# Kernel tuning notes

Hardware: AMD Instinct MI355X
Metric: run time of the kernel (lower is better)

The kernel has to match this reference:

```python
import jax, jax.numpy as jnp
import numpy as np

EPS = 1e-5
GROUPS = 8

def group_norm(x, w, b):
    B, C, H, W = x.shape
    xg = x.reshape(B, GROUPS, C // GROUPS, H, W)
    mean = xg.mean(axis=(2, 3, 4), keepdims=True)
    var = xg.var(axis=(2, 3, 4), keepdims=True)
    xn = ((xg - mean) * jax.lax.rsqrt(var + EPS)).reshape(B, C, H, W)
    return xn * w[None, :, None, None] + b[None, :, None, None]

def conv1x1(x, w, b):
    # x: [B,C,H,W], w: [O,C] -> [B,O,H,W]
    return jnp.einsum('bchw,oc->bohw', x, w) + b[None, :, None, None]

def setup_inputs() -> dict:
    key = jax.random.key(0)
    ks = jax.random.split(key, 16)
    C, Ci = 256, 128
    B, H, W = 4, 64, 64
    s3 = 1.0 / np.sqrt(C * 9)
    s1 = 1.0 / np.sqrt(C)
    return {
        'x': jax.random.normal(ks[0], (B, C, H, W), jnp.float32),
        'smooth_w': jax.random.uniform(ks[1], (C, C, 3, 3), jnp.float32, -s3, s3),
        'smooth_b': jax.random.uniform(ks[2], (C,), jnp.float32, -s3, s3),
        'gn1_w': jnp.ones((C,), jnp.float32),
        'gn1_b': jnp.zeros((C,), jnp.float32),
        'g_w': jax.random.uniform(ks[3], (Ci, C), jnp.float32, -s1, s1),
        'g_b': jax.random.uniform(ks[4], (Ci,), jnp.float32, -s1, s1),
        'theta_w': jax.random.uniform(ks[5], (Ci, C), jnp.float32, -s1, s1),
        'theta_b': jax.random.uniform(ks[6], (Ci,), jnp.float32, -s1, s1),
        'phi_w': jax.random.uniform(ks[7], (Ci, C), jnp.float32, -s1, s1),
        'phi_b': jax.random.uniform(ks[8], (Ci,), jnp.float32, -s1, s1),
        'w_w': 0.01 * jax.random.normal(ks[9], (C, Ci), jnp.float32),
        'w_b': jnp.zeros((C,), jnp.float32),
        'gn2_w': jnp.ones((C,), jnp.float32),
        'gn2_b': jnp.zeros((C,), jnp.float32),
    }

def reference(x, smooth_w, smooth_b, gn1_w, gn1_b, g_w, g_b, theta_w, theta_b,
              phi_w, phi_b, w_w, w_b, gn2_w, gn2_b):
    # input_smooth: 3x3 conv + GroupNorm(8) + ReLU
    xs = jax.lax.conv_general_dilated(
        x, smooth_w, window_strides=(1, 1), padding='SAME',
        dimension_numbers=('NCHW', 'OIHW', 'NCHW')) + smooth_b[None, :, None, None]
    xs = jax.nn.relu(group_norm(xs, gn1_w, gn1_b))
    B, C, H, W = xs.shape
    Ci = g_w.shape[0]
    N = H * W
    g_x = conv1x1(xs, g_w, g_b).reshape(B, Ci, N).transpose(0, 2, 1)      # [B,N,Ci]
    theta_x = conv1x1(xs, theta_w, theta_b).reshape(B, Ci, N).transpose(0, 2, 1)  # [B,N,Ci]
    phi_x = conv1x1(xs, phi_w, phi_b).reshape(B, Ci, N)                   # [B,Ci,N]
    f = jnp.einsum('bnc,bcm->bnm', theta_x, phi_x)                        # [B,N,N]
    attn = jax.nn.softmax(f, axis=-1)
    y = jnp.einsum('bnm,bmc->bnc', attn, g_x)                             # [B,N,Ci]
    y = y.transpose(0, 2, 1).reshape(B, Ci, H, W)
    w_y = group_norm(conv1x1(y, w_w, w_b), gn2_w, gn2_b)
    return w_y * 0.1 + xs
```

## Files before the change

### kernel.cpp

```cpp
#include <hip/hip_runtime.h>
#include <math.h>

#define Bn 4
#define Cn 256
#define CIn 128
#define Hn 64
#define Wn 64
#define Nn 4096
#define Gn 8
#define CPGn 32
#define EPSc 1e-5f

typedef unsigned short ushort_t;
typedef short bfrag __attribute__((ext_vector_type(8)));
typedef float f32x4 __attribute__((ext_vector_type(4)));
typedef ushort_t u16x8 __attribute__((ext_vector_type(8)));

static __device__ __forceinline__ ushort_t f2bf(float f) {
  unsigned u = __float_as_uint(f);
  return (ushort_t)((u + 0x7FFFu + ((u >> 16) & 1u)) >> 16);
}

static __device__ __forceinline__ unsigned cvt_pk_bf16(float lo, float hi) {
  unsigned r;
  asm("v_cvt_pk_bf16_f32 %0, %1, %2" : "=v"(r) : "v"(lo), "v"(hi));
  return r;
}

static __device__ __forceinline__ void gl_lds16(const ushort_t* g, ushort_t* l) {
  __builtin_amdgcn_global_load_lds(
      (__attribute__((address_space(1))) void*)g,
      (__attribute__((address_space(3))) void*)l, 16, 0, 0);
}

__global__ __launch_bounds__(256) void k_prepack(
    const float* __restrict__ w3, const float* __restrict__ thw,
    const float* __restrict__ phw, const float* __restrict__ gww,
    const float* __restrict__ ww,
    ushort_t* __restrict__ w9, ushort_t* __restrict__ wp9,
    ushort_t* __restrict__ wwb) {
  int i = blockIdx.x * 256 + threadIdx.x;
  if (i < 589824) {
    float v = w3[i];
    int co = i / 2304, r = i % 2304, ci = r / 9, tap = r % 9;
    w9[tap * 65536 + co * 256 + ci] = f2bf(v);
  } else if (i < 688128) {
    int j = i - 589824;
    int which = j >> 15, r = j & 32767;
    const float* src = (which == 0) ? thw : (which == 1) ? phw : gww;
    wp9[j] = f2bf(src[r]);
  } else if (i < 720896) {
    int j = i - 688128;
    wwb[j] = f2bf(ww[j]);
  }
}

__global__ __launch_bounds__(512) void k_conv_mfma(
    const float* __restrict__ x, const ushort_t* __restrict__ w9,
    const float* __restrict__ b3, float* __restrict__ out) {
  __shared__ __align__(16) ushort_t lx[3 * 66 * 128];
  const int tid = threadIdx.x;
  const int lane = tid & 63, w = tid >> 6;
  const int ln = lane & 15, lhi = lane >> 4;
  const int h = blockIdx.x, b = blockIdx.y;
  const int wco = w * 32;

  f32x4 acc[2][4];
#pragma unroll
  for (int mf = 0; mf < 2; ++mf)
#pragma unroll
    for (int nf = 0; nf < 4; ++nf) acc[mf][nf] = (f32x4){0.f, 0.f, 0.f, 0.f};

  for (int cc = 0; cc < 2; ++cc) {
    __syncthreads();
    for (int i = tid; i < 768; i += 512) {
      int dh = i / 256, r = i % 256, wpz = (r >> 7) ? 65 : 0, ci = r & 127;
      int off = (((dh * 66 + wpz) * 128 + ci) * 2) ^ ((wpz & 7) << 4);
      *(ushort_t*)((char*)lx + off) = 0;
    }
    for (int i = tid; i < 6144; i += 512) {
      int dh = i >> 11, r = i & 2047, ci = r >> 4, w4 = (r & 15) * 4;
      int hh = h + dh - 1;
      float4 v = {0.f, 0.f, 0.f, 0.f};
      if (hh >= 0 && hh < Hn)
        v = *(const float4*)(x + (((size_t)(b * Cn + cc * 128 + ci)) * Hn + hh) * Wn + w4);
      float vv[4] = {v.x, v.y, v.z, v.w};
#pragma unroll
      for (int j = 0; j < 4; ++j) {
        int wp = 1 + w4 + j;
        int off = (((dh * 66 + wp) * 128 + ci) * 2) ^ ((wp & 7) << 4);
        *(ushort_t*)((char*)lx + off) = f2bf(vv[j]);
      }
    }
    __syncthreads();

#pragma unroll
    for (int tap = 0; tap < 9; ++tap) {
      const int dh = tap / 3, dw = tap % 3;
#pragma unroll
      for (int kb = 0; kb < 4; ++kb) {
        const ushort_t* ap = w9 + tap * 65536 + (size_t)(wco + ln) * 256 +
                             cc * 128 + kb * 32 + lhi * 8;
        bfrag af0 = *(const bfrag*)ap;
        bfrag af1 = *(const bfrag*)(ap + 16 * 256);
        __builtin_amdgcn_s_setprio(1);
#pragma unroll
        for (int nf = 0; nf < 4; ++nf) {
          int wp = nf * 16 + ln + dw;
          int off = (((dh * 66 + wp) * 128 + kb * 32 + lhi * 8) * 2) ^ ((wp & 7) << 4);
          bfrag bf = *(const bfrag*)((const char*)lx + off);
          acc[0][nf] = __builtin_amdgcn_mfma_f32_16x16x32_bf16(af0, bf, acc[0][nf], 0, 0, 0);
          acc[1][nf] = __builtin_amdgcn_mfma_f32_16x16x32_bf16(af1, bf, acc[1][nf], 0, 0, 0);
        }
        __builtin_amdgcn_s_setprio(0);
      }
    }
  }

#pragma unroll
  for (int mf = 0; mf < 2; ++mf) {
    float4 bv = *(const float4*)(b3 + wco + mf * 16 + lhi * 4);
    float bb[4] = {bv.x, bv.y, bv.z, bv.w};
#pragma unroll
    for (int nf = 0; nf < 4; ++nf) {
#pragma unroll
      for (int r = 0; r < 4; ++r) {
        int co = wco + mf * 16 + lhi * 4 + r;
        out[((size_t)(b * Cn + co)) * Nn + h * Wn + nf * 16 + ln] = acc[mf][nf][r] + bb[r];
      }
    }
  }
}

__global__ __launch_bounds__(256) void k_gn_part(
    const float* __restrict__ xin, float* __restrict__ part) {
  const int s = blockIdx.x, g = blockIdx.y, b = blockIdx.z;
  const int t = threadIdx.x;
  const float* p = xin + ((size_t)b * Cn + g * CPGn) * Nn + s * 8192;
  float sum = 0.f, ssq = 0.f;
  for (int i = t * 4; i < 8192; i += 1024) {
    float4 v = *(const float4*)(p + i);
    sum += v.x + v.y + v.z + v.w;
    ssq += v.x * v.x + v.y * v.y + v.z * v.z + v.w * v.w;
  }
  __shared__ float r1[256], r2[256];
  r1[t] = sum; r2[t] = ssq;
  __syncthreads();
  for (int st = 128; st > 0; st >>= 1) {
    if (t < st) { r1[t] += r1[t + st]; r2[t] += r2[t + st]; }
    __syncthreads();
  }
  if (t == 0) {
    size_t idx = ((size_t)(b * Gn + g) * 16 + s) * 2;
    part[idx] = r1[0];
    part[idx + 1] = r2[0];
  }
}

__global__ void k_gn_final(const float* __restrict__ part, float* __restrict__ stats) {
  const int t = threadIdx.x;
  if (t < Bn * Gn) {
    float s = 0.f, ss = 0.f;
    for (int j = 0; j < 16; ++j) {
      s += part[(t * 16 + j) * 2];
      ss += part[(t * 16 + j) * 2 + 1];
    }
    const float inv = 1.f / (float)(CPGn * Nn);
    float mean = s * inv;
    float var = ss * inv - mean * mean;
    stats[t * 2] = mean;
    stats[t * 2 + 1] = rsqrtf(var + EPSc);
  }
}

__global__ __launch_bounds__(256) void k_gn1_apply_t(
    const float* __restrict__ xr, const float* __restrict__ stats,
    const float* __restrict__ gw, const float* __restrict__ gb,
    float* __restrict__ xs, ushort_t* __restrict__ xsT) {
  __shared__ ushort_t lt[32 * 64];
  const int t = threadIdx.x;
  const int n0 = blockIdx.x * 64, c0 = blockIdx.y * 32, b = blockIdx.z;
#pragma unroll
  for (int p = 0; p < 8; ++p) {
    int c = c0 + p * 4 + (t >> 6);
    int n = n0 + (t & 63);
    int bg = b * Gn + (c >> 5);
    float mean = stats[bg * 2], rstd = stats[bg * 2 + 1];
    float sc = gw[c] * rstd;
    float sb = gb[c] - mean * sc;
    size_t idx = ((size_t)(b * Cn + c)) * Nn + n;
    float val = fmaxf(xr[idx] * sc + sb, 0.f);
    xs[idx] = val;
    lt[(c - c0) * 64 + (t & 63)] = f2bf(val);
  }
  __syncthreads();
  {
    int n = t >> 2, cg = t & 3;
    u16x8 pk;
#pragma unroll
    for (int j = 0; j < 8; ++j) pk[j] = lt[(cg * 8 + j) * 64 + n];
    *(u16x8*)(xsT + ((size_t)(b * Nn + n0 + n)) * Cn + c0 + cg * 8) = pk;
  }
}

__global__ __launch_bounds__(256) void k_proj_mfma(
    const ushort_t* __restrict__ xsT, const ushort_t* __restrict__ wp9,
    const float* __restrict__ thb, const float* __restrict__ phb,
    const float* __restrict__ gbb,
    ushort_t* __restrict__ theta_b, ushort_t* __restrict__ phi_b,
    ushort_t* __restrict__ g_b) {
  __shared__ __align__(16) ushort_t lxs[64 * 256];
  const int tid = threadIdx.x;
  const int lane = tid & 63, w = tid >> 6;
  const int ln = lane & 15, lhi = lane >> 4;
  const int n0 = blockIdx.x * 64, which = blockIdx.y, b = blockIdx.z;
  const int wci = w * 32;

  for (int i = tid; i < 2048; i += 256) {
    int n = i >> 5, cchunk = (i & 31) * 8;
    uint4 v = *(const uint4*)(xsT + ((size_t)(b * Nn + n0 + n)) * Cn + cchunk);
    int off = ((n * 256 + cchunk) * 2) ^ ((n & 7) << 4);
    *(uint4*)((char*)lxs + off) = v;
  }
  __syncthreads();

  f32x4 acc[2][4];
#pragma unroll
  for (int mf = 0; mf < 2; ++mf)
#pragma unroll
    for (int nf = 0; nf < 4; ++nf) acc[mf][nf] = (f32x4){0.f, 0.f, 0.f, 0.f};

#pragma unroll
  for (int kb = 0; kb < 8; ++kb) {
    const ushort_t* ap = wp9 + which * 32768 + (size_t)(wci + ln) * 256 + kb * 32 + lhi * 8;
    bfrag af0 = *(const bfrag*)ap;
    bfrag af1 = *(const bfrag*)(ap + 16 * 256);
    __builtin_amdgcn_s_setprio(1);
#pragma unroll
    for (int nf = 0; nf < 4; ++nf) {
      int n = nf * 16 + ln;
      int off = ((n * 256 + kb * 32 + lhi * 8) * 2) ^ ((n & 7) << 4);
      bfrag bf = *(const bfrag*)((const char*)lxs + off);
      acc[0][nf] = __builtin_amdgcn_mfma_f32_16x16x32_bf16(af0, bf, acc[0][nf], 0, 0, 0);
      acc[1][nf] = __builtin_amdgcn_mfma_f32_16x16x32_bf16(af1, bf, acc[1][nf], 0, 0, 0);
    }
    __builtin_amdgcn_s_setprio(0);
  }

  const float* bs = (which == 0) ? thb : (which == 1) ? phb : gbb;
#pragma unroll
  for (int mf = 0; mf < 2; ++mf) {
    float4 bv = *(const float4*)(bs + wci + mf * 16 + lhi * 4);
    float bb[4] = {bv.x, bv.y, bv.z, bv.w};
    if (which < 2) {
      ushort_t* ob = ((which == 0) ? theta_b : phi_b) + (size_t)b * Nn * CIn;
#pragma unroll
      for (int nf = 0; nf < 4; ++nf) {
        int n = n0 + nf * 16 + ln;
        unsigned lo = (unsigned)f2bf(acc[mf][nf][0] + bb[0]) |
                      ((unsigned)f2bf(acc[mf][nf][1] + bb[1]) << 16);
        unsigned hi = (unsigned)f2bf(acc[mf][nf][2] + bb[2]) |
                      ((unsigned)f2bf(acc[mf][nf][3] + bb[3]) << 16);
        ushort_t* base = ob + (size_t)n * CIn + wci + mf * 16 + lhi * 4;
        *(unsigned*)base = lo;
        *(unsigned*)(base + 2) = hi;
      }
    } else {
      ushort_t* ob = g_b + (size_t)b * CIn * Nn;
#pragma unroll
      for (int nf = 0; nf < 4; ++nf) {
#pragma unroll
        for (int r = 0; r < 4; ++r) {
          int ci = wci + mf * 16 + lhi * 4 + r;
          ob[(size_t)ci * Nn + n0 + nf * 16 + ln] = f2bf(acc[mf][nf][r] + bb[r]);
        }
      }
    }
  }
}

__global__ __launch_bounds__(256) void k_attn_split(
    const ushort_t* __restrict__ theta_b, const ushort_t* __restrict__ phi_b,
    const ushort_t* __restrict__ g_b, ushort_t* __restrict__ ypart,
    float* __restrict__ mpart, float* __restrict__ lpart) {
  __shared__ __align__(16) ushort_t lphi[64 * 128];
  __shared__ __align__(16) ushort_t lg[128 * 64];
  __shared__ __align__(16) ushort_t lP[4][16 * 64];

  const int tid = threadIdx.x;
  const int lane = tid & 63, w = tid >> 6;
  const int ln = lane & 15, lhi = lane >> 4;

  const int bid = blockIdx.x;
  const int xcd = bid & 7, idx = bid >> 3;
  const int pair = xcd * 2 + (idx >> 6);
  const int b = pair >> 2, s = pair & 3;
  const int n0 = (idx & 63) * 64;
  const int kv0 = s * 1024;

  bfrag qf[4];
  {
    const ushort_t* thp =
        theta_b + ((size_t)(b * Nn + n0 + w * 16 + ln)) * CIn + 8 * lhi;
#pragma unroll
    for (int kb = 0; kb < 4; ++kb) qf[kb] = *(const bfrag*)(thp + kb * 32);
  }

  f32x4 yacc[8];
#pragma unroll
  for (int df = 0; df < 8; ++df) yacc[df] = (f32x4){0.f, 0.f, 0.f, 0.f};
  float mq = -3e38f, lq = 0.f;

  const ushort_t* gphi[4];
  const ushort_t* gg[4];
  ushort_t* ldphi[4];
  ushort_t* ldg[4];
#pragma unroll
  for (int k = 0; k < 4; ++k) {
    int ch = w * 4 + k;
    int boff = ch * 1024 + lane * 16;
    {
      int m = boff >> 8, c = (boff >> 4) & 15, cp = c ^ (m & 7);
      gphi[k] = phi_b + (size_t)b * Nn * CIn + (size_t)(kv0 + m) * CIn + cp * 8;
      ldphi[k] = lphi + ch * 512;
    }
    {
      int d = boff >> 7, c = (boff >> 4) & 7, cp = c ^ (d & 7);
      gg[k] = g_b + (size_t)b * CIn * Nn + (size_t)d * Nn + kv0 + cp * 8;
      ldg[k] = lg + ch * 512;
    }
  }
#pragma unroll
  for (int k = 0; k < 4; ++k) {
    gl_lds16(gphi[k], ldphi[k]);
    gl_lds16(gg[k], ldg[k]);
  }

  ushort_t* lPw = lP[w];

  for (int t = 0; t < 16; ++t) {
    __syncthreads();

    f32x4 sacc[4];
#pragma unroll
    for (int nf = 0; nf < 4; ++nf) sacc[nf] = (f32x4){0.f, 0.f, 0.f, 0.f};
    __builtin_amdgcn_s_setprio(1);
#pragma unroll
    for (int kb = 0; kb < 4; ++kb) {
#pragma unroll
      for (int nf = 0; nf < 4; ++nf) {
        int row = nf * 16 + ln;
        int off = ((row * 128 + kb * 32 + 8 * lhi) * 2) ^ ((ln & 7) << 4);
        bfrag pf = *(const bfrag*)((const char*)lphi + off);
        sacc[nf] = __builtin_amdgcn_mfma_f32_16x16x32_bf16(pf, qf[kb], sacc[nf], 0, 0, 0);
      }
    }
    __builtin_amdgcn_s_setprio(0);

    float mx;
    {
      float a0 = fmaxf(fmaxf(sacc[0][0], sacc[0][1]), fmaxf(sacc[0][2], sacc[0][3]));
      float a1 = fmaxf(fmaxf(sacc[1][0], sacc[1][1]), fmaxf(sacc[1][2], sacc[1][3]));
      float a2 = fmaxf(fmaxf(sacc[2][0], sacc[2][1]), fmaxf(sacc[2][2], sacc[2][3]));
      float a3 = fmaxf(fmaxf(sacc[3][0], sacc[3][1]), fmaxf(sacc[3][2], sacc[3][3]));
      mx = fmaxf(fmaxf(a0, a1), fmaxf(a2, a3));
    }
    mx = fmaxf(mx, __shfl_xor(mx, 16));
    mx = fmaxf(mx, __shfl_xor(mx, 32));
    float nm = fmaxf(mq, mx);
    float aaq = __expf(mq - nm);
    mq = nm;

    float psum = 0.f;
#pragma unroll
    for (int nf = 0; nf < 4; ++nf) {
      float p0 = __expf(sacc[nf][0] - nm);
      float p1 = __expf(sacc[nf][1] - nm);
      float p2 = __expf(sacc[nf][2] - nm);
      float p3 = __expf(sacc[nf][3] - nm);
      psum += (p0 + p1) + (p2 + p3);
      uint2 pk;
      pk.x = cvt_pk_bf16(p0, p1);
      pk.y = cvt_pk_bf16(p2, p3);
      int off = ((ln * 64 + nf * 16 + lhi * 4) * 2) ^ ((ln & 7) << 4);
      *(uint2*)((char*)lPw + off) = pk;
    }
    psum += __shfl_xor(psum, 16);
    psum += __shfl_xor(psum, 32);
    lq = lq * aaq + psum;

    float aar[4];
#pragma unroll
    for (int r = 0; r < 4; ++r) aar[r] = __shfl(aaq, 4 * lhi + r);
#pragma unroll
    for (int df = 0; df < 8; ++df)
#pragma unroll
      for (int r = 0; r < 4; ++r) yacc[df][r] *= aar[r];

    __builtin_amdgcn_s_setprio(1);
#pragma unroll
    for (int kb2 = 0; kb2 < 2; ++kb2) {
      int offa = ((ln * 64 + kb2 * 32 + 8 * lhi) * 2) ^ ((ln & 7) << 4);
      bfrag pa = *(const bfrag*)((const char*)lPw + offa);
#pragma unroll
      for (int df = 0; df < 8; ++df) {
        int d = df * 16 + ln;
        int offb = ((d * 64 + kb2 * 32 + 8 * lhi) * 2) ^ ((ln & 7) << 4);
        bfrag gbf = *(const bfrag*)((const char*)lg + offb);
        yacc[df] = __builtin_amdgcn_mfma_f32_16x16x32_bf16(pa, gbf, yacc[df], 0, 0, 0);
      }
    }
    __builtin_amdgcn_s_setprio(0);

    __syncthreads();
    if (t < 15) {
#pragma unroll
      for (int k = 0; k < 4; ++k) {
        gphi[k] += 64 * CIn;
        gg[k] += 64;
        gl_lds16(gphi[k], ldphi[k]);
        gl_lds16(gg[k], ldg[k]);
      }
    }
  }

  {
    ushort_t* ly = lphi;
#pragma unroll
    for (int df = 0; df < 8; ++df) {
#pragma unroll
      for (int r = 0; r < 4; ++r) {
        int q = w * 16 + lhi * 4 + r;
        int off = ((q * 128 + df * 16 + ln) * 2) ^ ((q & 7) << 4);
        *(ushort_t*)((char*)ly + off) = f2bf(yacc[df][r]);
      }
    }
  }
  __syncthreads();
  {
    int q = tid >> 2, c0 = (tid & 3) * 32;
    ushort_t* yp = ypart + ((size_t)((b * 4 + s) * Nn + n0 + q)) * CIn + c0;
#pragma unroll
    for (int k = 0; k < 4; ++k) {
      int off = ((q * 128 + c0 + k * 8) * 2) ^ ((q & 7) << 4);
      uint4 v = *(const uint4*)((const char*)lphi + off);
      *(uint4*)(yp + k * 8) = v;
    }
  }
  if (lhi == 0) {
    size_t qi = (size_t)(b * 4 + s) * Nn + n0 + w * 16 + ln;
    mpart[qi] = mq;
    lpart[qi] = lq;
  }
}

__global__ __launch_bounds__(256) void k_merge(
    const ushort_t* __restrict__ ypart, const float* __restrict__ mpart,
    const float* __restrict__ lpart, ushort_t* __restrict__ yT) {
  const int t = threadIdx.x;
  const int n = blockIdx.x * 64 + (t >> 2);
  const int b = blockIdx.y;
  const int d0 = (t & 3) * 32;
  float m[4], l[4];
#pragma unroll
  for (int s = 0; s < 4; ++s) {
    m[s] = mpart[(size_t)(b * 4 + s) * Nn + n];
    l[s] = lpart[(size_t)(b * 4 + s) * Nn + n];
  }
  float M = fmaxf(fmaxf(m[0], m[1]), fmaxf(m[2], m[3]));
  float L = 0.f, sc[4];
#pragma unroll
  for (int s = 0; s < 4; ++s) { sc[s] = __expf(m[s] - M); L += sc[s] * l[s]; }
  float inv = 1.f / L;
  float acc[32];
#pragma unroll
  for (int k = 0; k < 32; ++k) acc[k] = 0.f;
#pragma unroll
  for (int s = 0; s < 4; ++s) {
    const ushort_t* yp = ypart + ((size_t)((b * 4 + s) * Nn + n)) * CIn + d0;
#pragma unroll
    for (int k = 0; k < 4; ++k) {
      u16x8 v = *(const u16x8*)(yp + k * 8);
#pragma unroll
      for (int j = 0; j < 8; ++j)
        acc[k * 8 + j] += sc[s] * __uint_as_float((unsigned)v[j] << 16);
    }
  }
  ushort_t* op = yT + ((size_t)(b * Nn + n)) * CIn + d0;
#pragma unroll
  for (int k = 0; k < 4; ++k) {
    u16x8 pk;
#pragma unroll
    for (int j = 0; j < 8; ++j) pk[j] = f2bf(acc[k * 8 + j] * inv);
    *(u16x8*)(op + k * 8) = pk;
  }
}

__global__ __launch_bounds__(512) void k_wconv_mfma(
    const ushort_t* __restrict__ yT, const ushort_t* __restrict__ wwb,
    const float* __restrict__ wb, float* __restrict__ wy) {
  __shared__ __align__(16) ushort_t lyt[64 * 128];
  const int tid = threadIdx.x;
  const int lane = tid & 63, w = tid >> 6;
  const int ln = lane & 15, lhi = lane >> 4;
  const int n0 = blockIdx.x * 64, b = blockIdx.y;
  const int wco = w * 32;

  for (int i = tid; i < 1024; i += 512) {
    int n = i >> 4, ch = (i & 15) * 8;
    uint4 v = *(const uint4*)(yT + ((size_t)(b * Nn + n0 + n)) * CIn + ch);
    int off = ((n * 128 + ch) * 2) ^ ((n & 7) << 4);
    *(uint4*)((char*)lyt + off) = v;
  }
  __syncthreads();

  f32x4 acc[2][4];
#pragma unroll
  for (int mf = 0; mf < 2; ++mf)
#pragma unroll
    for (int nf = 0; nf < 4; ++nf) acc[mf][nf] = (f32x4){0.f, 0.f, 0.f, 0.f};

#pragma unroll
  for (int kb = 0; kb < 4; ++kb) {
    const ushort_t* ap = wwb + (size_t)(wco + ln) * CIn + kb * 32 + lhi * 8;
    bfrag af0 = *(const bfrag*)ap;
    bfrag af1 = *(const bfrag*)(ap + 16 * CIn);
    __builtin_amdgcn_s_setprio(1);
#pragma unroll
    for (int nf = 0; nf < 4; ++nf) {
      int n = nf * 16 + ln;
      int off = ((n * 128 + kb * 32 + lhi * 8) * 2) ^ ((n & 7) << 4);
      bfrag bf = *(const bfrag*)((const char*)lyt + off);
      acc[0][nf] = __builtin_amdgcn_mfma_f32_16x16x32_bf16(af0, bf, acc[0][nf], 0, 0, 0);
      acc[1][nf] = __builtin_amdgcn_mfma_f32_16x16x32_bf16(af1, bf, acc[1][nf], 0, 0, 0);
    }
    __builtin_amdgcn_s_setprio(0);
  }

#pragma unroll
  for (int mf = 0; mf < 2; ++mf) {
    float4 bv = *(const float4*)(wb + wco + mf * 16 + lhi * 4);
    float bb[4] = {bv.x, bv.y, bv.z, bv.w};
#pragma unroll
    for (int nf = 0; nf < 4; ++nf) {
#pragma unroll
      for (int r = 0; r < 4; ++r) {
        int co = wco + mf * 16 + lhi * 4 + r;
        wy[((size_t)(b * Cn + co)) * Nn + n0 + nf * 16 + ln] = acc[mf][nf][r] + bb[r];
      }
    }
  }
}

__global__ __launch_bounds__(256) void k_final(
    const float* __restrict__ wy, const float* __restrict__ stats,
    const float* __restrict__ g2w, const float* __restrict__ g2b,
    const float* __restrict__ xs, float* __restrict__ out) {
  size_t i = ((size_t)blockIdx.x * 256 + threadIdx.x) * 4;
  int c = (int)((i >> 12) & 255);
  int bg = (int)(i >> 20) * Gn + (c >> 5);
  float mean = stats[bg * 2], rstd = stats[bg * 2 + 1];
  float sc = g2w[c] * rstd * 0.1f;
  float sb = (g2b[c] - mean * rstd * g2w[c]) * 0.1f;
  float4 v = *(const float4*)(wy + i);
  float4 xv = *(const float4*)(xs + i);
  v.x = v.x * sc + sb + xv.x;
  v.y = v.y * sc + sb + xv.y;
  v.z = v.z * sc + sb + xv.z;
  v.w = v.w * sc + sb + xv.w;
  *(float4*)(out + i) = v;
}

extern "C" void kernel_launch(void* const* d_in, const int* in_sizes, int n_in,
                              void* d_out, int out_size, void* d_ws, size_t ws_size,
                              hipStream_t stream) {
  (void)in_sizes; (void)n_in; (void)out_size; (void)ws_size;
  const float* x   = (const float*)d_in[0];
  const float* sw  = (const float*)d_in[1];
  const float* sb  = (const float*)d_in[2];
  const float* g1w = (const float*)d_in[3];
  const float* g1b = (const float*)d_in[4];
  const float* gw  = (const float*)d_in[5];
  const float* gb  = (const float*)d_in[6];
  const float* thw = (const float*)d_in[7];
  const float* thb = (const float*)d_in[8];
  const float* phw = (const float*)d_in[9];
  const float* phb = (const float*)d_in[10];
  const float* ww  = (const float*)d_in[11];
  const float* wb  = (const float*)d_in[12];
  const float* g2w = (const float*)d_in[13];
  const float* g2b = (const float*)d_in[14];
  float* out = (float*)d_out;
  float* ws = (float*)d_ws;

  float*    xs_raw  = ws;
  float*    xs      = ws + 4194304;
  ushort_t* yT      = (ushort_t*)(ws + 8388608);
  float*    part    = ws + 10485760;
  float*    st1     = ws + 10486784;
  float*    st2     = ws + 10486848;
  ushort_t* theta_b = (ushort_t*)(ws + 10486912);
  ushort_t* phi_b   = (ushort_t*)(ws + 11535488);
  ushort_t* g_b     = (ushort_t*)(ws + 12584064);
  ushort_t* xsT     = (ushort_t*)(ws + 13632640);
  ushort_t* w9      = (ushort_t*)(ws + 15729792);
  ushort_t* wp9     = (ushort_t*)(ws + 16024704);
  ushort_t* wwb     = (ushort_t*)(ws + 16073856);
  ushort_t* ypart   = (ushort_t*)xs_raw;
  float*    mpart   = (float*)xsT;
  float*    lpart   = ((float*)xsT) + 65536;
  float*    wy      = xs_raw;

  k_prepack<<<2816, 256, 0, stream>>>(sw, thw, phw, gw, ww, w9, wp9, wwb);
  k_conv_mfma<<<dim3(Hn, Bn), 512, 0, stream>>>(x, w9, sb, xs_raw);
  k_gn_part<<<dim3(16, 8, 4), 256, 0, stream>>>(xs_raw, part);
  k_gn_final<<<1, 64, 0, stream>>>(part, st1);
  k_gn1_apply_t<<<dim3(64, 8, 4), 256, 0, stream>>>(xs_raw, st1, g1w, g1b, xs, xsT);
  k_proj_mfma<<<dim3(64, 3, 4), 256, 0, stream>>>(xsT, wp9, thb, phb, gb,
                                                  theta_b, phi_b, g_b);
  k_attn_split<<<1024, 256, 0, stream>>>(theta_b, phi_b, g_b, ypart, mpart, lpart);
  k_merge<<<dim3(64, 4), 256, 0, stream>>>(ypart, mpart, lpart, yT);
  k_wconv_mfma<<<dim3(64, 4), 512, 0, stream>>>(yT, wwb, wb, wy);
  k_gn_part<<<dim3(16, 8, 4), 256, 0, stream>>>(wy, part);
  k_gn_final<<<1, 64, 0, stream>>>(part, st2);
  k_final<<<4096, 256, 0, stream>>>(wy, st2, g2w, g2b, xs, out);
}
```

Measured before the change: 181.9 us.

## Fuse GroupNorm partial stats into conv epilogues and merge into wconv

Group-norm partial sums and sums of squares are now computed in the epilogues of the 3x3 conv and the output 1x1 conv, using wave shuffles. This removes the two separate k_gn_part passes that re-read full fp32 activations. The flash-split merge kernel is folded into k_wconv_mfma, which combines the four bf16 partial outputs with softmax rescale factors while staging into LDS, so the yT round trip goes away. Buffers are reassigned in the workspace to avoid aliasing, and k_gn_final now reduces 64 partials per group instead of 16.

Result: faster. 168.1 us (median of 2 runs) (-7.6%).

```diff
diff --git a/kernel.cpp b/kernel.cpp
--- a/kernel.cpp
+++ b/kernel.cpp
@@ -25,6 +25,10 @@
   unsigned r;
   asm("v_cvt_pk_bf16_f32 %0, %1, %2" : "=v"(r) : "v"(lo), "v"(hi));
   return r;
+}
+
+static __device__ __forceinline__ float bf2f(ushort_t u) {
+  return __uint_as_float((unsigned)u << 16);
 }
 
 static __device__ __forceinline__ void gl_lds16(const ushort_t* g, ushort_t* l) {
@@ -57,7 +61,8 @@
 
 __global__ __launch_bounds__(512) void k_conv_mfma(
     const float* __restrict__ x, const ushort_t* __restrict__ w9,
-    const float* __restrict__ b3, float* __restrict__ out) {
+    const float* __restrict__ b3, float* __restrict__ out,
+    float* __restrict__ part) {
   __shared__ __align__(16) ushort_t lx[3 * 66 * 128];
   const int tid = threadIdx.x;
   const int lane = tid & 63, w = tid >> 6;
@@ -117,6 +122,7 @@
     }
   }
 
+  float s_ = 0.f, q_ = 0.f;
 #pragma unroll
   for (int mf = 0; mf < 2; ++mf) {
     float4 bv = *(const float4*)(b3 + wco + mf * 16 + lhi * 4);
@@ -126,34 +132,22 @@
 #pragma unroll
       for (int r = 0; r < 4; ++r) {
         int co = wco + mf * 16 + lhi * 4 + r;
-        out[((size_t)(b * Cn + co)) * Nn + h * Wn + nf * 16 + ln] = acc[mf][nf][r] + bb[r];
-      }
-    }
-  }
-}
-
-__global__ __launch_bounds__(256) void k_gn_part(
-    const float* __restrict__ xin, float* __restrict__ part) {
-  const int s = blockIdx.x, g = blockIdx.y, b = blockIdx.z;
-  const int t = threadIdx.x;
-  const float* p = xin + ((size_t)b * Cn + g * CPGn) * Nn + s * 8192;
-  float sum = 0.f, ssq = 0.f;
-  for (int i = t * 4; i < 8192; i += 1024) {
-    float4 v = *(const float4*)(p + i);
-    sum += v.x + v.y + v.z + v.w;
-    ssq += v.x * v.x + v.y * v.y + v.z * v.z + v.w * v.w;
-  }
-  __shared__ float r1[256], r2[256];
-  r1[t] = sum; r2[t] = ssq;
-  __syncthreads();
-  for (int st = 128; st > 0; st >>= 1) {
-    if (t < st) { r1[t] += r1[t + st]; r2[t] += r2[t + st]; }
-    __syncthreads();
-  }
-  if (t == 0) {
-    size_t idx = ((size_t)(b * Gn + g) * 16 + s) * 2;
-    part[idx] = r1[0];
-    part[idx + 1] = r2[0];
+        float v = acc[mf][nf][r] + bb[r];
+        out[((size_t)(b * Cn + co)) * Nn + h * Wn + nf * 16 + ln] = v;
+        s_ += v;
+        q_ += v * v;
+      }
+    }
+  }
+#pragma unroll
+  for (int off = 32; off; off >>= 1) {
+    s_ += __shfl_xor(s_, off);
+    q_ += __shfl_xor(q_, off);
+  }
+  if (lane == 0) {
+    size_t pi = ((size_t)(b * Gn + w) * 64 + h) * 2;
+    part[pi] = s_;
+    part[pi + 1] = q_;
   }
 }
 
@@ -161,9 +155,9 @@
   const int t = threadIdx.x;
   if (t < Bn * Gn) {
     float s = 0.f, ss = 0.f;
-    for (int j = 0; j < 16; ++j) {
-      s += part[(t * 16 + j) * 2];
-      ss += part[(t * 16 + j) * 2 + 1];
+    for (int j = 0; j < 64; ++j) {
+      s += part[(t * 64 + j) * 2];
+      ss += part[(t * 64 + j) * 2 + 1];
     }
     const float inv = 1.f / (float)(CPGn * Nn);
     float mean = s * inv;
@@ -454,63 +448,55 @@
   }
 }
 
-__global__ __launch_bounds__(256) void k_merge(
+__global__ __launch_bounds__(512) void k_wconv_mfma(
     const ushort_t* __restrict__ ypart, const float* __restrict__ mpart,
-    const float* __restrict__ lpart, ushort_t* __restrict__ yT) {
-  const int t = threadIdx.x;
-  const int n = blockIdx.x * 64 + (t >> 2);
-  const int b = blockIdx.y;
-  const int d0 = (t & 3) * 32;
-  float m[4], l[4];
-#pragma unroll
-  for (int s = 0; s < 4; ++s) {
-    m[s] = mpart[(size_t)(b * 4 + s) * Nn + n];
-    l[s] = lpart[(size_t)(b * 4 + s) * Nn + n];
-  }
-  float M = fmaxf(fmaxf(m[0], m[1]), fmaxf(m[2], m[3]));
-  float L = 0.f, sc[4];
-#pragma unroll
-  for (int s = 0; s < 4; ++s) { sc[s] = __expf(m[s] - M); L += sc[s] * l[s]; }
-  float inv = 1.f / L;
-  float acc[32];
-#pragma unroll
-  for (int k = 0; k < 32; ++k) acc[k] = 0.f;
-#pragma unroll
-  for (int s = 0; s < 4; ++s) {
-    const ushort_t* yp = ypart + ((size_t)((b * 4 + s) * Nn + n)) * CIn + d0;
-#pragma unroll
-    for (int k = 0; k < 4; ++k) {
-      u16x8 v = *(const u16x8*)(yp + k * 8);
-#pragma unroll
-      for (int j = 0; j < 8; ++j)
-        acc[k * 8 + j] += sc[s] * __uint_as_float((unsigned)v[j] << 16);
-    }
-  }
-  ushort_t* op = yT + ((size_t)(b * Nn + n)) * CIn + d0;
-#pragma unroll
-  for (int k = 0; k < 4; ++k) {
-    u16x8 pk;
-#pragma unroll
-    for (int j = 0; j < 8; ++j) pk[j] = f2bf(acc[k * 8 + j] * inv);
-    *(u16x8*)(op + k * 8) = pk;
-  }
-}
-
-__global__ __launch_bounds__(512) void k_wconv_mfma(
-    const ushort_t* __restrict__ yT, const ushort_t* __restrict__ wwb,
-    const float* __restrict__ wb, float* __restrict__ wy) {
+    const float* __restrict__ lpart, const ushort_t* __restrict__ wwb,
+    const float* __restrict__ wb, float* __restrict__ wy,
+    float* __restrict__ part) {
   __shared__ __align__(16) ushort_t lyt[64 * 128];
+  __shared__ float fSc[4][64];
   const int tid = threadIdx.x;
   const int lane = tid & 63, w = tid >> 6;
   const int ln = lane & 15, lhi = lane >> 4;
   const int n0 = blockIdx.x * 64, b = blockIdx.y;
   const int wco = w * 32;
 
+  if (tid < 64) {
+    int n = n0 + tid;
+    float m0 = mpart[(size_t)(b * 4 + 0) * Nn + n], l0 = lpart[(size_t)(b * 4 + 0) * Nn + n];
+    float m1 = mpart[(size_t)(b * 4 + 1) * Nn + n], l1 = lpart[(size_t)(b * 4 + 1) * Nn + n];
+    float m2 = mpart[(size_t)(b * 4 + 2) * Nn + n], l2 = lpart[(size_t)(b * 4 + 2) * Nn + n];
+    float m3 = mpart[(size_t)(b * 4 + 3) * Nn + n], l3 = lpart[(size_t)(b * 4 + 3) * Nn + n];
+    float M = fmaxf(fmaxf(m0, m1), fmaxf(m2, m3));
+    float s0 = __expf(m0 - M), s1 = __expf(m1 - M), s2 = __expf(m2 - M), s3 = __expf(m3 - M);
+    float inv = 1.f / (s0 * l0 + s1 * l1 + s2 * l2 + s3 * l3);
+    fSc[0][tid] = s0 * inv;
+    fSc[1][tid] = s1 * inv;
+    fSc[2][tid] = s2 * inv;
+    fSc[3][tid] = s3 * inv;
+  }
+  __syncthreads();
+
   for (int i = tid; i < 1024; i += 512) {
     int n = i >> 4, ch = (i & 15) * 8;
-    uint4 v = *(const uint4*)(yT + ((size_t)(b * Nn + n0 + n)) * CIn + ch);
+    float f0 = fSc[0][n], f1 = fSc[1][n], f2 = fSc[2][n], f3 = fSc[3][n];
+    const ushort_t* yb = ypart + ((size_t)(b * 4) * Nn + n0 + n) * CIn + ch;
+    const size_t sstr = (size_t)Nn * CIn;
+    u16x8 v0 = *(const u16x8*)(yb);
+    u16x8 v1 = *(const u16x8*)(yb + sstr);
+    u16x8 v2 = *(const u16x8*)(yb + 2 * sstr);
+    u16x8 v3 = *(const u16x8*)(yb + 3 * sstr);
+    float a[8];
+#pragma unroll
+    for (int j = 0; j < 8; ++j)
+      a[j] = f0 * bf2f(v0[j]) + f1 * bf2f(v1[j]) + f2 * bf2f(v2[j]) + f3 * bf2f(v3[j]);
+    uint4 pk;
+    pk.x = cvt_pk_bf16(a[0], a[1]);
+    pk.y = cvt_pk_bf16(a[2], a[3]);
+    pk.z = cvt_pk_bf16(a[4], a[5]);
+    pk.w = cvt_pk_bf16(a[6], a[7]);
     int off = ((n * 128 + ch) * 2) ^ ((n & 7) << 4);
-    *(uint4*)((char*)lyt + off) = v;
+    *(uint4*)((char*)lyt + off) = pk;
   }
   __syncthreads();
 
@@ -537,6 +523,7 @@
     __builtin_amdgcn_s_setprio(0);
   }
 
+  float s_ = 0.f, q_ = 0.f;
 #pragma unroll
   for (int mf = 0; mf < 2; ++mf) {
     float4 bv = *(const float4*)(wb + wco + mf * 16 + lhi * 4);
@@ -546,9 +533,22 @@
 #pragma unroll
       for (int r = 0; r < 4; ++r) {
         int co = wco + mf * 16 + lhi * 4 + r;
-        wy[((size_t)(b * Cn + co)) * Nn + n0 + nf * 16 + ln] = acc[mf][nf][r] + bb[r];
-      }
-    }
+        float v = acc[mf][nf][r] + bb[r];
+        wy[((size_t)(b * Cn + co)) * Nn + n0 + nf * 16 + ln] = v;
+        s_ += v;
+        q_ += v * v;
+      }
+    }
+  }
+#pragma unroll
+  for (int off = 32; off; off >>= 1) {
+    s_ += __shfl_xor(s_, off);
+    q_ += __shfl_xor(q_, off);
+  }
+  if (lane == 0) {
+    size_t pi = ((size_t)(b * Gn + w) * 64 + blockIdx.x) * 2;
+    part[pi] = s_;
+    part[pi + 1] = q_;
   }
 }
 
@@ -595,10 +595,6 @@
 
   float*    xs_raw  = ws;
   float*    xs      = ws + 4194304;
-  ushort_t* yT      = (ushort_t*)(ws + 8388608);
-  float*    part    = ws + 10485760;
-  float*    st1     = ws + 10486784;
-  float*    st2     = ws + 10486848;
   ushort_t* theta_b = (ushort_t*)(ws + 10486912);
   ushort_t* phi_b   = (ushort_t*)(ws + 11535488);
   ushort_t* g_b     = (ushort_t*)(ws + 12584064);
@@ -606,22 +602,22 @@
   ushort_t* w9      = (ushort_t*)(ws + 15729792);
   ushort_t* wp9     = (ushort_t*)(ws + 16024704);
   ushort_t* wwb     = (ushort_t*)(ws + 16073856);
+  float*    wy      = ws + 10486912;
   ushort_t* ypart   = (ushort_t*)xs_raw;
-  float*    mpart   = (float*)xsT;
-  float*    lpart   = ((float*)xsT) + 65536;
-  float*    wy      = xs_raw;
+  float*    mpart   = ws + 16090240;
+  float*    lpart   = ws + 16155776;
+  float*    part    = ws + 16221312;
+  float*    st1     = ws + 16225408;
+  float*    st2     = ws + 16225472;
 
   k_prepack<<<2816, 256, 0, stream>>>(sw, thw, phw, gw, ww, w9, wp9, wwb);
-  k_conv_mfma<<<dim3(Hn, Bn), 512, 0, stream>>>(x, w9, sb, xs_raw);
-  k_gn_part<<<dim3(16, 8, 4), 256, 0, stream>>>(xs_raw, part);
+  k_conv_mfma<<<dim3(Hn, Bn), 512, 0, stream>>>(x, w9, sb, xs_raw, part);
   k_gn_final<<<1, 64, 0, stream>>>(part, st1);
   k_gn1_apply_t<<<dim3(64, 8, 4), 256, 0, stream>>>(xs_raw, st1, g1w, g1b, xs, xsT);
   k_proj_mfma<<<dim3(64, 3, 4), 256, 0, stream>>>(xsT, wp9, thb, phb, gb,
                                                   theta_b, phi_b, g_b);
   k_attn_split<<<1024, 256, 0, stream>>>(theta_b, phi_b, g_b, ypart, mpart, lpart);
-  k_merge<<<dim3(64, 4), 256, 0, stream>>>(ypart, mpart, lpart, yT);
-  k_wconv_mfma<<<dim3(64, 4), 512, 0, stream>>>(yT, wwb, wb, wy);
-  k_gn_part<<<dim3(16, 8, 4), 256, 0, stream>>>(wy, part);
+  k_wconv_mfma<<<dim3(64, 4), 512, 0, stream>>>(ypart, mpart, lpart, wwb, wb, wy, part);
   k_gn_final<<<1, 64, 0, stream>>>(part, st2);
   k_final<<<4096, 256, 0, stream>>>(wy, st2, g2w, g2b, xs, out);
 }
```
